# Kernel tuning notes

Measured on AMD Instinct MI355X. Metric: run time of the kernel, lower is better.

The kernel has to match this reference:

```python
import jax, jax.numpy as jnp
import numpy as np
from jax import lax

RADIUS = 0.15
K = 32          # num_neighbors
S = 1024        # num_centers
GROUPS = 8      # GroupNorm groups
EPS = 1e-5


def furthest_point_sample(xyz, n_samples):
    # xyz: [B, N, 3] -> indices [B, n_samples] (sequential FPS, start at index 0)
    B, N, _ = xyz.shape
    def step(carry, _):
        min_d, far = carry                      # [B,N], [B]
        sel = jnp.take_along_axis(xyz, far[:, None, None], axis=1)  # [B,1,3]
        d = jnp.sum((xyz - sel) ** 2, axis=-1)  # [B,N]
        min_d = jnp.minimum(min_d, d)
        nxt = jnp.argmax(min_d, axis=-1).astype(jnp.int32)
        return (min_d, nxt), far
    init = (jnp.full((B, N), jnp.inf, dtype=xyz.dtype), jnp.zeros((B,), jnp.int32))
    _, idxs = lax.scan(step, init, None, length=n_samples)  # [n_samples, B]
    return idxs.T  # [B, n_samples]


def ball_query(centers, points, radius, k):
    # centers: [B,3,S], points: [B,3,N] -> neighbor indices [B,S,k]
    B = points.shape[0]
    N = points.shape[-1]
    d2 = jnp.sum((centers[:, :, :, None] - points[:, :, None, :]) ** 2, axis=1)  # [B,S,N]
    valid = d2 < radius * radius
    order = jnp.where(valid, jnp.arange(N, dtype=jnp.int32), jnp.int32(N))
    topk = jnp.sort(order, axis=-1)[..., :k]            # first-k in-ball indices (CUDA ball_query order)
    first = topk[..., :1]
    idx = jnp.where(topk < N, topk, first)              # pad shortfall with first in-ball point
    idx = jnp.where(idx == N, 0, idx)                   # empty ball -> index 0
    return idx


def grouping(x, idx):
    # x: [B,C,N], idx: [B,S,k] -> [B,C,S,k]
    B, C, N = x.shape
    _, s, k = idx.shape
    flat = idx.reshape(B, 1, s * k)
    g = jnp.take_along_axis(x, jnp.broadcast_to(flat, (B, C, s * k)), axis=2)
    return g.reshape(B, C, s, k)


def group_norm(x, gamma, beta):
    # x: [B,C,S,K], GroupNorm(GROUPS)
    B, C, s, k = x.shape
    xg = x.reshape(B, GROUPS, C // GROUPS, s, k)
    mu = jnp.mean(xg, axis=(2, 3, 4), keepdims=True)
    var = jnp.var(xg, axis=(2, 3, 4), keepdims=True)
    xn = ((xg - mu) * lax.rsqrt(var + EPS)).reshape(B, C, s, k)
    return xn * gamma[None, :, None, None] + beta[None, :, None, None]


def mlp_layer(x, w, b, gamma, beta):
    # 1x1 Conv2d + GroupNorm + swish; x: [B,C,S,K], w: [O,C]
    y = jnp.einsum('bcsk,oc->bosk', x, w) + b[None, :, None, None]
    y = group_norm(y, gamma, beta)
    return y * jax.nn.sigmoid(y)


def setup_inputs() -> dict:
    key = jax.random.key(0)
    ks = jax.random.split(key, 20)
    B, C_IN, N = 8, 128, 4096
    features = jax.random.normal(ks[0], (B, C_IN, N), jnp.float32)
    coords = jax.random.uniform(ks[1], (B, 3, N), jnp.float32)
    time_emb = jax.random.normal(ks[2], (B, 64, N), jnp.float32)
    style = jax.random.normal(ks[3], (B, 64), jnp.float32)
    chans = [C_IN + 3, 128, 128, 256]
    inp = dict(features=features, coords=coords, time_emb=time_emb, style=style)
    for i in range(3):
        ci, co = chans[i], chans[i + 1]
        inp[f'w{i+1}'] = jax.random.normal(ks[4 + 4 * i], (co, ci), jnp.float32) / np.sqrt(ci)
        inp[f'b{i+1}'] = jnp.zeros((co,), jnp.float32)
        inp[f'g{i+1}'] = jnp.ones((co,), jnp.float32)
        inp[f'be{i+1}'] = jnp.zeros((co,), jnp.float32)
    return inp


def reference(features, coords, time_emb, style,
              w1, b1, g1, be1, w2, b2, g2, be2, w3, b3, g3, be3):
    # FPS -> center coords
    fps_idx = furthest_point_sample(coords.transpose(0, 2, 1), S)       # [B,S]
    B = coords.shape[0]
    centers = jnp.take_along_axis(coords, jnp.broadcast_to(fps_idx[:, None, :], (B, 3, S)), axis=2)  # [B,3,S]
    # Ball query + grouping (include_coordinates=True)
    nidx = ball_query(centers, coords, RADIUS, K)                       # [B,S,K]
    ncoords = grouping(coords, nidx) - centers[:, :, :, None]           # [B,3,S,K]
    nfeat = jnp.concatenate([ncoords, grouping(features, nidx)], axis=1)  # [B,3+C,S,K]
    # SharedMLP (1x1 conv + GN(8) + swish) x3, then max over neighbors
    x = mlp_layer(nfeat, w1, b1, g1, be1)
    x = mlp_layer(x, w2, b2, g2, be2)
    x = mlp_layer(x, w3, b3, g3, be3)
    out = jnp.max(x, axis=-1)                                           # [B,256,S]
    return out, centers, time_emb[:, :, :S], style
```

## Files before the change

kernel.cpp:

```cpp
#include <hip/hip_runtime.h>
#include <hip/hip_bf16.h>

#define BATCH 8
#define NPTS 4096
#define NS   1024
#define NK   32
#define CIN  128
#define C1PAD 160
#define O1   128
#define O3   256
#define MTOT 32768
#define GN_EPS 1e-5f

typedef float f32x4 __attribute__((ext_vector_type(4)));
typedef float f32x2 __attribute__((ext_vector_type(2)));
typedef short s16x8 __attribute__((ext_vector_type(8)));
typedef short s16x4 __attribute__((ext_vector_type(4)));
typedef unsigned long long u64;
typedef u64 u64x2 __attribute__((ext_vector_type(2)));

static __device__ __forceinline__ unsigned short f2bf(float f){
  unsigned u = __float_as_uint(f);
  u += 0x7fffu + ((u >> 16) & 1u);
  return (unsigned short)(u >> 16);
}
static __device__ __forceinline__ float bf2f(unsigned short h){
  return __uint_as_float(((unsigned)h) << 16);
}
static __device__ __forceinline__ float exact_d2(float ax,float ay,float az,float bx,float by,float bz){
  float dx=__fadd_rn(ax,-bx), dy=__fadd_rn(ay,-by), dz=__fadd_rn(az,-bz);
  return __fadd_rn(__fadd_rn(__fmul_rn(dx,dx),__fmul_rn(dy,dy)),__fmul_rn(dz,dz));
}
static __device__ __forceinline__ unsigned wave_umax_dpp(unsigned v){
  unsigned o;
  o = (unsigned)__builtin_amdgcn_update_dpp(0, (int)v, 0x111, 0xf, 0xf, true); v = (o>v)?o:v;
  o = (unsigned)__builtin_amdgcn_update_dpp(0, (int)v, 0x112, 0xf, 0xf, true); v = (o>v)?o:v;
  o = (unsigned)__builtin_amdgcn_update_dpp(0, (int)v, 0x114, 0xf, 0xf, true); v = (o>v)?o:v;
  o = (unsigned)__builtin_amdgcn_update_dpp(0, (int)v, 0x118, 0xf, 0xf, true); v = (o>v)?o:v;
  o = (unsigned)__builtin_amdgcn_update_dpp(0, (int)v, 0x142, 0xf, 0xf, true); v = (o>v)?o:v;
  o = (unsigned)__builtin_amdgcn_update_dpp(0, (int)v, 0x143, 0xf, 0xf, true); v = (o>v)?o:v;
  return v;
}
static __device__ __forceinline__ float wave_fsum_dpp(float v){
  int o;
  o=__builtin_amdgcn_update_dpp(0,__float_as_int(v),0x111,0xf,0xf,true); v+=__int_as_float(o);
  o=__builtin_amdgcn_update_dpp(0,__float_as_int(v),0x112,0xf,0xf,true); v+=__int_as_float(o);
  o=__builtin_amdgcn_update_dpp(0,__float_as_int(v),0x114,0xf,0xf,true); v+=__int_as_float(o);
  o=__builtin_amdgcn_update_dpp(0,__float_as_int(v),0x118,0xf,0xf,true); v+=__int_as_float(o);
  o=__builtin_amdgcn_update_dpp(0,__float_as_int(v),0x142,0xf,0xf,true); v+=__int_as_float(o);
  o=__builtin_amdgcn_update_dpp(0,__float_as_int(v),0x143,0xf,0xf,true); v+=__int_as_float(o);
  return v;
}
static __device__ __forceinline__ float fast_sigmoid(float x){
  return __builtin_amdgcn_rcpf(1.0f + __expf(-x));
}

#define FPS_BLOCKS 8
#define FT_BASE    8
#define FT_BLOCKS  128
#define ZP_BASE    136
#define ZP_BLOCKS  8
#define WP_BASE    144
#define WP_BLOCKS  36
#define MS_BASE    180
#define MS_BLOCKS  32
#define TOTAL_BLOCKS 212

__global__ __launch_bounds__(256) void k_fused(
    const float* __restrict__ coords, const float* __restrict__ features,
    const float* __restrict__ time_emb, const float* __restrict__ style,
    const float* __restrict__ w1, const float* __restrict__ w2, const float* __restrict__ w3,
    float* __restrict__ centers, float* __restrict__ out_time, float* __restrict__ out_style,
    unsigned short* __restrict__ featT, unsigned short* __restrict__ wfrag,
    float* __restrict__ stats){
  union U {
    struct { float4 lc[NPTS];
             unsigned long long red[2][4] __attribute__((aligned(16))); } fps;
    float tile[64][65];
  };
  __shared__ U sm;
  const int blk = blockIdx.x;
  const int t = threadIdx.x;

  if(blk < FPS_BLOCKS){
    const int b = blk;
    const float* cb = coords + (size_t)b*3*NPTS;
    const int lane = t & 63, wid = t >> 6;
    f32x2 px2[8],py2[8],pz2[8],md2[8];
    #pragma unroll
    for(int i=0;i<8;++i){
      int p0 = t + (2*i)*256;
      px2[i]=(f32x2){cb[p0],cb[p0+256]};
      py2[i]=(f32x2){cb[NPTS+p0],cb[NPTS+p0+256]};
      pz2[i]=(f32x2){cb[2*NPTS+p0],cb[2*NPTS+p0+256]};
      md2[i]=(f32x2){3.4e38f,3.4e38f};
      sm.fps.lc[p0]     = make_float4(px2[i].x, py2[i].x, pz2[i].x, 0.f);
      sm.fps.lc[p0+256] = make_float4(px2[i].y, py2[i].y, pz2[i].y, 0.f);
    }
    float ax=cb[0], ay=cb[NPTS], az=cb[2*NPTS];
    if(t==0){
      centers[(size_t)(b*3+0)*NS]=ax;
      centers[(size_t)(b*3+1)*NS]=ay;
      centers[(size_t)(b*3+2)*NS]=az;
    }
    __syncthreads();
    for(int it=1; it<NS; ++it){
      {
        #pragma clang fp contract(off)
        f32x2 axv={ax,ax}, ayv={ay,ay}, azv={az,az};
        #pragma unroll
        for(int i=0;i<8;++i){
          f32x2 dx=px2[i]-axv, dy=py2[i]-ayv, dz=pz2[i]-azv;
          f32x2 d = dx*dx + dy*dy + dz*dz;
          md2[i].x=fminf(md2[i].x,d.x);
          md2[i].y=fminf(md2[i].y,d.y);
        }
      }
      float m[8];
      #pragma unroll
      for(int i=0;i<8;++i) m[i]=fmaxf(md2[i].x,md2[i].y);
      float bmax=fmaxf(fmaxf(fmaxf(m[0],m[1]),fmaxf(m[2],m[3])),
                       fmaxf(fmaxf(m[4],m[5]),fmaxf(m[6],m[7])));
      unsigned bvb=(unsigned)__builtin_amdgcn_readlane((int)wave_umax_dpp(__float_as_uint(bmax)),63);
      unsigned cand=0u;
      #pragma unroll
      for(int s=15;s>=0;--s){
        float mv = (s&1)? md2[s>>1].y : md2[s>>1].x;
        cand = (__float_as_uint(mv)==bvb) ? ~(unsigned)(s*256+t) : cand;
      }
      unsigned mc = wave_umax_dpp(cand);
      const int buf=it&1;
      if(lane==63) sm.fps.red[buf][wid] = ((u64)bvb<<32) | mc;
      __syncthreads();
      u64x2 r0 = *(const u64x2*)&sm.fps.red[buf][0];
      u64x2 r1 = *(const u64x2*)&sm.fps.red[buf][2];
      u64 a0 = r0.x>r0.y?r0.x:r0.y;
      u64 a1 = r1.x>r1.y?r1.x:r1.y;
      u64 w  = a0>a1?a0:a1;
      unsigned idx = ~(unsigned)w;
      float4 c4 = sm.fps.lc[idx];
      ax=c4.x; ay=c4.y; az=c4.z;
      if(t==0){
        centers[(size_t)(b*3+0)*NS+it]=ax;
        centers[(size_t)(b*3+1)*NS+it]=ay;
        centers[(size_t)(b*3+2)*NS+it]=az;
      }
    }
    return;
  }

  if(blk < ZP_BASE){
    const int pb = blk - FT_BASE;
    for(int j=0;j<8;++j){
      int tid = pb*8 + j;
      int bb = tid>>7, r = tid&127, ct = r>>6, pt = r&63;
      int c0 = ct*64, p0 = pt*64;
      #pragma unroll
      for(int i=0;i<16;++i){
        int c = (t>>6)*16 + i;
        sm.tile[c][t&63] = features[((size_t)bb*CIN + c0 + c)*NPTS + p0 + (t&63)];
      }
      __syncthreads();
      #pragma unroll
      for(int i=0;i<16;++i){
        int pl = (t>>6)*16 + i;
        featT[((size_t)bb*NPTS + p0 + pl)*C1PAD + c0 + (t&63)] = f2bf(sm.tile[t&63][pl]);
      }
      __syncthreads();
    }
    return;
  }

  if(blk < WP_BASE){
    const int zb = blk - ZP_BASE;
    s16x8 z = (s16x8){0,0,0,0,0,0,0,0};
    #pragma unroll 4
    for(int i=0;i<64;++i){
      int q = zb*16384 + i*256 + t;
      int bb = q>>14, rem = q&16383, r = rem>>2, c8 = (rem&3)*8;
      *(s16x8*)&featT[((size_t)bb*NPTS + r)*C1PAD + 128 + c8] = z;
    }
    return;
  }

  if(blk < MS_BASE){
    int task = (blk - WP_BASE)*256 + t;
    if(task >= 9088) return;
    if(task >= 8704){
      int z = task - 8704;
      if(z < 3*BATCH*8*2) stats[z] = 0.f;
      return;
    }
    int layer, of, cs, ln, ncs; size_t base;
    if(task < 2560){ layer=0; ncs=5; base=0;     int r=task;      of=r/320; r%=320; cs=r>>6; ln=r&63; }
    else if(task < 4608){ layer=1; ncs=4; base=20480; int r=task-2560; of=r>>8; r&=255; cs=r>>6; ln=r&63; }
    else { layer=2; ncs=4; base=36864; int r=task-4608; of=r>>8; r&=255; cs=r>>6; ln=r&63; }
    int o = of*16 + (ln&15);
    s16x8 vals;
    #pragma unroll
    for(int i=0;i<8;++i){
      int c = cs*32 + (ln>>4)*8 + i;
      float v = 0.f;
      if(layer==0){
        if(c<128) v = w1[o*131 + c + 3];
        else if(c<131) v = w1[o*131 + (c-128)];
      } else if(layer==1){
        if(c<128) v = w2[o*128 + c];
      } else {
        if(c<128) v = w3[o*128 + c];
      }
      vals[i]=(short)f2bf(v);
    }
    *(s16x8*)&wfrag[base + ((size_t)(of*ncs + cs)*64 + ln)*8] = vals;
    return;
  }

  {
    const int mb = blk - MS_BASE;
    #pragma unroll 4
    for(int i=0;i<16;++i){
      int q = mb*4096 + i*256 + t;
      int f = q*4;
      int bb = f>>16, c = (f>>10)&63, s = f&1023;
      *(float4*)&out_time[f] = *(const float4*)&time_emb[((size_t)bb*64 + c)*NPTS + s];
    }
    if(mb==0){ out_style[t]=style[t]; out_style[256+t]=style[256+t]; }
  }
}

__global__ __launch_bounds__(256) void k_ballq(const float* __restrict__ coords,
                                               const float* __restrict__ centers,
                                               int* __restrict__ nidx){
  const int gw = (blockIdx.x*256 + threadIdx.x) >> 6;
  const int lane = threadIdx.x & 63;
  const int wl = (threadIdx.x >> 6);
  const int b = gw >> 10, s = gw & (NS-1);
  const float* cb = coords + (size_t)b*3*NPTS;
  const float cx = centers[(size_t)(b*3+0)*NS+s];
  const float cy = centers[(size_t)(b*3+1)*NS+s];
  const float cz = centers[(size_t)(b*3+2)*NS+s];
  __shared__ int slots[4][NK];
  int cnt = 0;
  for(int base=0; base<NPTS && cnt<NK; base+=64){
    int p = base + lane;
    float d2 = exact_d2(cb[p], cb[NPTS+p], cb[2*NPTS+p], cx,cy,cz);
    bool valid = d2 < 0.0225f;
    unsigned long long mask = __ballot(valid);
    int pos = cnt + (int)__popcll(mask & ((1ull<<lane)-1ull));
    if(valid && pos < NK) slots[wl][pos] = p;
    cnt += (int)__popcll(mask);
  }
  __syncthreads();
  int first = slots[wl][0];
  if(lane < NK){
    int v = (lane < cnt) ? slots[wl][lane] : first;
    nidx[((size_t)b*NS + s)*NK + lane] = v;
  }
}

__global__ __launch_bounds__(256) void k_gemm1(const unsigned short* __restrict__ featT,
    const int* __restrict__ nidx, const float* __restrict__ coords,
    const float* __restrict__ centers, const unsigned short* __restrict__ wfrag,
    const float* __restrict__ bias, unsigned short* __restrict__ yout,
    float* __restrict__ stats){
  const int b=blockIdx.y, mt=blockIdx.x;
  const int m0=mt*64;
  const int t=threadIdx.x, lane=t&63, wid=t>>6;
  __shared__ unsigned short xs[64][168];
  __shared__ unsigned short ys[64][136];
  __shared__ int pidx[64];
  __shared__ float cenS[2][3];
  __shared__ float wsum[2][8][4];
  if(t<64) pidx[t]=nidx[(size_t)b*MTOT + m0 + t];
  if(t>=64 && t<70){ int u=t-64; int j=u/3, c=u%3; cenS[j][c]=centers[((size_t)b*3+c)*NS + (m0>>5)+j]; }
  __syncthreads();
  for(int q=t;q<1280;q+=256){
    int r=q&63, ch=q>>6;
    *(s16x8*)&xs[r][ch*8] = *(const s16x8*)&featT[((size_t)b*NPTS + pidx[r])*C1PAD + ch*8];
  }
  __syncthreads();
  if(t<64){
    int p=pidx[t]; int sj=t>>5;
    float n0=__fadd_rn(coords[((size_t)b*3+0)*NPTS+p],-cenS[sj][0]);
    float n1=__fadd_rn(coords[((size_t)b*3+1)*NPTS+p],-cenS[sj][1]);
    float n2=__fadd_rn(coords[((size_t)b*3+2)*NPTS+p],-cenS[sj][2]);
    s16x4 nc={(short)f2bf(n0),(short)f2bf(n1),(short)f2bf(n2),0};
    *(s16x4*)&xs[t][128]=nc;
  }
  __syncthreads();
  f32x4 acc[8];
  #pragma unroll
  for(int i=0;i<8;++i) acc[i]=(f32x4){0.f,0.f,0.f,0.f};
  const unsigned short* xrow=&xs[wid*16+(lane&15)][0];
  #pragma unroll
  for(int cs=0;cs<5;++cs){
    s16x8 bfv=*(const s16x8*)&xrow[cs*32+(lane>>4)*8];
    #pragma unroll
    for(int of=0;of<8;++of){
      s16x8 afv=*(const s16x8*)&wfrag[((size_t)(of*5+cs)*64+lane)*8];
      acc[of]=__builtin_amdgcn_mfma_f32_16x16x32_bf16(afv,bfv,acc[of],0,0,0);
    }
  }
  #pragma unroll
  for(int of=0;of<8;++of){
    float ls=0.f,lq=0.f;
    int obase=of*16+((lane>>4)<<2);
    #pragma unroll
    for(int r=0;r<4;++r){
      float y=acc[of][r]+bias[obase+r];
      ys[wid*16+(lane&15)][obase+r]=f2bf(y);
      ls+=y; lq+=y*y;
    }
    ls=wave_fsum_dpp(ls); lq=wave_fsum_dpp(lq);
    if(lane==63){ wsum[0][of][wid]=ls; wsum[1][of][wid]=lq; }
  }
  __syncthreads();
  for(int q=t;q<1024;q+=256){
    int r=q&63, ch=q>>6;
    *(s16x8*)&yout[((size_t)b*MTOT+m0+r)*O1 + ch*8] = *(const s16x8*)&ys[r][ch*8];
  }
  if(t<8){
    float s1v=wsum[0][t][0]+wsum[0][t][1]+wsum[0][t][2]+wsum[0][t][3];
    float s2v=wsum[1][t][0]+wsum[1][t][1]+wsum[1][t][2]+wsum[1][t][3];
    atomicAdd(&stats[((0*BATCH+b)*8+t)*2+0],s1v);
    atomicAdd(&stats[((0*BATCH+b)*8+t)*2+1],s2v);
  }
}

template<int LAYER>
__global__ __launch_bounds__(256) void k_gemm23(const unsigned short* __restrict__ xin,
    const unsigned short* __restrict__ wfrag, const float* __restrict__ bias,
    const float* __restrict__ stats, const float* __restrict__ gprev,
    const float* __restrict__ beprev, unsigned short* __restrict__ yout,
    float* __restrict__ ymm, float* __restrict__ statsOut){
  const int b=blockIdx.y, mt=blockIdx.x;
  const int m0=mt*64;
  const int t=threadIdx.x, lane=t&63, wid=t>>6;
  __shared__ unsigned short xs[64][136];
  __shared__ unsigned short ys[64][136];
  __shared__ float lsc[CIN], lsh[CIN];
  __shared__ float wsum[2][8][4];
  if(t<CIN){
    int g = t>>4;
    const float cnt = 16.0f*NS*NK;
    float s1=stats[(((LAYER-1)*BATCH+b)*8+g)*2+0];
    float s2=stats[(((LAYER-1)*BATCH+b)*8+g)*2+1];
    float mu=s1/cnt, var=s2/cnt-mu*mu;
    float sc=gprev[t]*rsqrtf(var+GN_EPS);
    lsc[t]=sc; lsh[t]=beprev[t]-mu*sc;
  }
  __syncthreads();
  for(int q=t;q<1024;q+=256){
    int r=q&63, ch=q>>6;
    s16x8 v = *(const s16x8*)&xin[((size_t)b*MTOT + m0 + r)*CIN + ch*8];
    s16x8 o;
    #pragma unroll
    for(int i=0;i<8;++i){
      int c=ch*8+i;
      float x = bf2f((unsigned short)v[i]);
      x = x*lsc[c] + lsh[c];
      o[i]=(short)f2bf(x*fast_sigmoid(x));
    }
    *(s16x8*)&xs[r][ch*8]=o;
  }
  __syncthreads();
  const unsigned short* xrow=&xs[wid*16+(lane&15)][0];
  s16x8 bfv[4];
  #pragma unroll
  for(int cs=0;cs<4;++cs) bfv[cs]=*(const s16x8*)&xrow[cs*32+(lane>>4)*8];
  const int NPH=(LAYER==2)?2:1;
  #pragma unroll
  for(int ph=0; ph<NPH; ++ph){
    f32x4 acc[8];
    #pragma unroll
    for(int i=0;i<8;++i) acc[i]=(f32x4){0.f,0.f,0.f,0.f};
    #pragma unroll
    for(int cs=0;cs<4;++cs){
      #pragma unroll
      for(int of=0;of<8;++of){
        int ofg=ph*8+of;
        s16x8 afv=*(const s16x8*)&wfrag[((size_t)(ofg*4+cs)*64+lane)*8];
        acc[of]=__builtin_amdgcn_mfma_f32_16x16x32_bf16(afv,bfv[cs],acc[of],0,0,0);
      }
    }
    #pragma unroll
    for(int of=0;of<8;++of){
      float ls=0.f,lq=0.f;
      int lobase=of*16+((lane>>4)<<2);
      #pragma unroll
      for(int r=0;r<4;++r){
        float y=acc[of][r]+bias[ph*128+lobase+r];
        ys[wid*16+(lane&15)][lobase+r]=f2bf(y);
        ls+=y; lq+=y*y;
      }
      ls=wave_fsum_dpp(ls); lq=wave_fsum_dpp(lq);
      if(lane==63){ wsum[0][of][wid]=ls; wsum[1][of][wid]=lq; }
    }
    __syncthreads();
    if constexpr(LAYER==1){
      for(int q=t;q<1024;q+=256){
        int r=q&63, ch=q>>6;
        *(s16x8*)&yout[((size_t)b*MTOT+m0+r)*O1 + ch*8] = *(const s16x8*)&ys[r][ch*8];
      }
    } else {
      int c = t&127, sg = t>>7;
      float mn=3.4e38f, mx=-3.4e38f;
      #pragma unroll 8
      for(int k=0;k<32;++k){
        float v = bf2f(ys[sg*32+k][c]);
        mn=fminf(mn,v); mx=fmaxf(mx,v);
      }
      *(float2*)&ymm[(((size_t)b*NS + mt*2 + sg)*512) + (size_t)(ph*128+c)*2] = make_float2(mn,mx);
    }
    if(t<8){
      float s1v=wsum[0][t][0]+wsum[0][t][1]+wsum[0][t][2]+wsum[0][t][3];
      float s2v=wsum[1][t][0]+wsum[1][t][1]+wsum[1][t][2]+wsum[1][t][3];
      int g = (LAYER==2) ? (ph*4 + (t>>1)) : t;
      atomicAdd(&statsOut[((LAYER*BATCH+b)*8+g)*2+0],s1v);
      atomicAdd(&statsOut[((LAYER*BATCH+b)*8+g)*2+1],s2v);
    }
    if(ph+1<NPH) __syncthreads();
  }
}

__global__ __launch_bounds__(256) void k_out(const float* __restrict__ ymm,
    const float* __restrict__ stats, const float* __restrict__ g3,
    const float* __restrict__ be3, float* __restrict__ out){
  const int b=blockIdx.z, st=blockIdx.x;
  const int t=threadIdx.x;
  __shared__ float outT[256][33];
  const int c=t, g=c>>5;
  const float cnt = 32.0f*NS*NK;
  float s1=stats[((2*BATCH+b)*8+g)*2+0];
  float s2=stats[((2*BATCH+b)*8+g)*2+1];
  float mu=s1/cnt, var=s2/cnt-mu*mu;
  float sc=g3[c]*rsqrtf(var+GN_EPS);
  float sh=be3[c]-mu*sc;
  for(int si=0;si<32;++si){
    int s=st*32+si;
    float2 v=*(const float2*)&ymm[((size_t)b*NS+s)*512 + (size_t)c*2];
    float za=v.x*sc+sh, zb=v.y*sc+sh;
    float fa=za*fast_sigmoid(za);
    float fb=zb*fast_sigmoid(zb);
    outT[c][si]=fmaxf(fa,fb);
  }
  __syncthreads();
  #pragma unroll
  for(int i=0;i<32;++i){
    int row=(t>>5)+i*8;
    out[((size_t)(b*256+row))*NS + st*32 + (t&31)] = outT[row][t&31];
  }
}

extern "C" void kernel_launch(void* const* d_in, const int* in_sizes, int n_in,
                              void* d_out, int out_size, void* d_ws, size_t ws_size,
                              hipStream_t stream){
  const float* features=(const float*)d_in[0];
  const float* coords=(const float*)d_in[1];
  const float* time_emb=(const float*)d_in[2];
  const float* style=(const float*)d_in[3];
  const float* w1=(const float*)d_in[4];
  const float* b1=(const float*)d_in[5];
  const float* g1=(const float*)d_in[6];
  const float* be1=(const float*)d_in[7];
  const float* w2=(const float*)d_in[8];
  const float* b2=(const float*)d_in[9];
  const float* g2=(const float*)d_in[10];
  const float* be2=(const float*)d_in[11];
  const float* w3=(const float*)d_in[12];
  const float* b3=(const float*)d_in[13];
  const float* g3=(const float*)d_in[14];
  const float* be3=(const float*)d_in[15];

  float* out0=(float*)d_out;
  float* out_centers=out0 + (size_t)BATCH*O3*NS;
  float* out_time=out_centers + (size_t)BATCH*3*NS;
  float* out_style=out_time + (size_t)BATCH*64*NS;

  char* ws=(char*)d_ws;
  int* nidx=(int*)(ws + 131072);
  unsigned short* featT=(unsigned short*)(ws + 1179648);
  unsigned short* wfrag=(unsigned short*)(ws + 11796480);
  float* stats=(float*)(ws + 11939840);
  float* ymm=(float*)(ws + 12582912);
  unsigned short* y1=(unsigned short*)(ws + 33554432);
  unsigned short* y2=(unsigned short*)(ws + 100663296);

  k_fused<<<TOTAL_BLOCKS,256,0,stream>>>(coords,features,time_emb,style,w1,w2,w3,
                                         out_centers,out_time,out_style,featT,wfrag,stats);
  k_ballq<<<2048,256,0,stream>>>(coords,out_centers,nidx);
  k_gemm1<<<dim3(512,BATCH),256,0,stream>>>(featT,nidx,coords,out_centers,wfrag,b1,y1,stats);
  k_gemm23<1><<<dim3(512,BATCH),256,0,stream>>>(y1,wfrag+20480,b2,stats,g1,be1,y2,ymm,stats);
  k_gemm23<2><<<dim3(512,BATCH),256,0,stream>>>(y2,wfrag+36864,b3,stats,g2,be2,y2,ymm,stats);
  k_out<<<dim3(32,1,BATCH),256,0,stream>>>(ymm,stats,g3,be3,out0);
}
```

Baseline: 1.051 ms.

## Fuse ball query into GEMM1, DPP min/max in layer 3, vectorize FPS min/max

The standalone ball-query kernel is removed. Two waves of each GEMM1 block now run the neighbor search for their own two centers and write the indices straight into shared memory, which drops a kernel launch and the global round trip for the index buffer. In layer 3, the per-neighbor min/max is computed with 16-lane DPP reductions on register values instead of writing bf16 tiles to LDS and scanning 32 rows. The FPS loop also switches to packed 2-wide elementwise min/max. The cost is that half the waves in each GEMM1 block do serial ball-query work while the other two wait at the barrier.

```diff
diff --git a/kernel.cpp b/kernel.cpp
--- a/kernel.cpp
+++ b/kernel.cpp
@@ -49,6 +49,22 @@
   o=__builtin_amdgcn_update_dpp(0,__float_as_int(v),0x118,0xf,0xf,true); v+=__int_as_float(o);
   o=__builtin_amdgcn_update_dpp(0,__float_as_int(v),0x142,0xf,0xf,true); v+=__int_as_float(o);
   o=__builtin_amdgcn_update_dpp(0,__float_as_int(v),0x143,0xf,0xf,true); v+=__int_as_float(o);
+  return v;
+}
+static __device__ __forceinline__ float grp16_fmin_dpp(float v){
+  int o;
+  o=__builtin_amdgcn_update_dpp(0,__float_as_int(v),0x111,0xf,0xf,true); v=fminf(v,__int_as_float(o));
+  o=__builtin_amdgcn_update_dpp(0,__float_as_int(v),0x112,0xf,0xf,true); v=fminf(v,__int_as_float(o));
+  o=__builtin_amdgcn_update_dpp(0,__float_as_int(v),0x114,0xf,0xf,true); v=fminf(v,__int_as_float(o));
+  o=__builtin_amdgcn_update_dpp(0,__float_as_int(v),0x118,0xf,0xf,true); v=fminf(v,__int_as_float(o));
+  return v;
+}
+static __device__ __forceinline__ float grp16_fmax_dpp(float v){
+  int o;
+  o=__builtin_amdgcn_update_dpp(0,__float_as_int(v),0x111,0xf,0xf,true); v=fmaxf(v,__int_as_float(o));
+  o=__builtin_amdgcn_update_dpp(0,__float_as_int(v),0x112,0xf,0xf,true); v=fmaxf(v,__int_as_float(o));
+  o=__builtin_amdgcn_update_dpp(0,__float_as_int(v),0x114,0xf,0xf,true); v=fmaxf(v,__int_as_float(o));
+  o=__builtin_amdgcn_update_dpp(0,__float_as_int(v),0x118,0xf,0xf,true); v=fmaxf(v,__int_as_float(o));
   return v;
 }
 static __device__ __forceinline__ float fast_sigmoid(float x){
@@ -112,15 +128,17 @@
         for(int i=0;i<8;++i){
           f32x2 dx=px2[i]-axv, dy=py2[i]-ayv, dz=pz2[i]-azv;
           f32x2 d = dx*dx + dy*dy + dz*dz;
-          md2[i].x=fminf(md2[i].x,d.x);
-          md2[i].y=fminf(md2[i].y,d.y);
+          md2[i]=__builtin_elementwise_min(md2[i],d);
         }
       }
-      float m[8];
-      #pragma unroll
-      for(int i=0;i<8;++i) m[i]=fmaxf(md2[i].x,md2[i].y);
-      float bmax=fmaxf(fmaxf(fmaxf(m[0],m[1]),fmaxf(m[2],m[3])),
-                       fmaxf(fmaxf(m[4],m[5]),fmaxf(m[6],m[7])));
+      f32x2 t01=__builtin_elementwise_max(md2[0],md2[1]);
+      f32x2 t23=__builtin_elementwise_max(md2[2],md2[3]);
+      f32x2 t45=__builtin_elementwise_max(md2[4],md2[5]);
+      f32x2 t67=__builtin_elementwise_max(md2[6],md2[7]);
+      f32x2 ta=__builtin_elementwise_max(t01,t23);
+      f32x2 tb=__builtin_elementwise_max(t45,t67);
+      f32x2 tc=__builtin_elementwise_max(ta,tb);
+      float bmax=fmaxf(tc.x,tc.y);
       unsigned bvb=(unsigned)__builtin_amdgcn_readlane((int)wave_umax_dpp(__float_as_uint(bmax)),63);
       unsigned cand=0u;
       #pragma unroll
@@ -228,41 +246,10 @@
   }
 }
 
-__global__ __launch_bounds__(256) void k_ballq(const float* __restrict__ coords,
-                                               const float* __restrict__ centers,
-                                               int* __restrict__ nidx){
-  const int gw = (blockIdx.x*256 + threadIdx.x) >> 6;
-  const int lane = threadIdx.x & 63;
-  const int wl = (threadIdx.x >> 6);
-  const int b = gw >> 10, s = gw & (NS-1);
-  const float* cb = coords + (size_t)b*3*NPTS;
-  const float cx = centers[(size_t)(b*3+0)*NS+s];
-  const float cy = centers[(size_t)(b*3+1)*NS+s];
-  const float cz = centers[(size_t)(b*3+2)*NS+s];
-  __shared__ int slots[4][NK];
-  int cnt = 0;
-  for(int base=0; base<NPTS && cnt<NK; base+=64){
-    int p = base + lane;
-    float d2 = exact_d2(cb[p], cb[NPTS+p], cb[2*NPTS+p], cx,cy,cz);
-    bool valid = d2 < 0.0225f;
-    unsigned long long mask = __ballot(valid);
-    int pos = cnt + (int)__popcll(mask & ((1ull<<lane)-1ull));
-    if(valid && pos < NK) slots[wl][pos] = p;
-    cnt += (int)__popcll(mask);
-  }
-  __syncthreads();
-  int first = slots[wl][0];
-  if(lane < NK){
-    int v = (lane < cnt) ? slots[wl][lane] : first;
-    nidx[((size_t)b*NS + s)*NK + lane] = v;
-  }
-}
-
 __global__ __launch_bounds__(256) void k_gemm1(const unsigned short* __restrict__ featT,
-    const int* __restrict__ nidx, const float* __restrict__ coords,
-    const float* __restrict__ centers, const unsigned short* __restrict__ wfrag,
-    const float* __restrict__ bias, unsigned short* __restrict__ yout,
-    float* __restrict__ stats){
+    const float* __restrict__ coords, const float* __restrict__ centers,
+    const unsigned short* __restrict__ wfrag, const float* __restrict__ bias,
+    unsigned short* __restrict__ yout, float* __restrict__ stats){
   const int b=blockIdx.y, mt=blockIdx.x;
   const int m0=mt*64;
   const int t=threadIdx.x, lane=t&63, wid=t>>6;
@@ -271,8 +258,29 @@
   __shared__ int pidx[64];
   __shared__ float cenS[2][3];
   __shared__ float wsum[2][8][4];
-  if(t<64) pidx[t]=nidx[(size_t)b*MTOT + m0 + t];
-  if(t>=64 && t<70){ int u=t-64; int j=u/3, c=u%3; cenS[j][c]=centers[((size_t)b*3+c)*NS + (m0>>5)+j]; }
+  if(wid<2){
+    const int s0=(m0>>5)+wid;
+    const float cx=centers[(size_t)(b*3+0)*NS+s0];
+    const float cy=centers[(size_t)(b*3+1)*NS+s0];
+    const float cz=centers[(size_t)(b*3+2)*NS+s0];
+    if(lane==0){ cenS[wid][0]=cx; cenS[wid][1]=cy; cenS[wid][2]=cz; }
+    const float* cb=coords+(size_t)b*3*NPTS;
+    int cnt=0;
+    for(int base=0;base<NPTS&&cnt<NK;base+=64){
+      int p=base+lane;
+      float d2=exact_d2(cb[p],cb[NPTS+p],cb[2*NPTS+p],cx,cy,cz);
+      bool valid=d2<0.0225f;
+      unsigned long long mask=__ballot(valid);
+      int pos=cnt+(int)__popcll(mask&((1ull<<lane)-1ull));
+      if(valid&&pos<NK) pidx[wid*32+pos]=p;
+      cnt+=(int)__popcll(mask);
+    }
+    int first=pidx[wid*32];
+    if(lane<NK){
+      int v=(lane<cnt)?pidx[wid*32+lane]:first;
+      pidx[wid*32+lane]=v;
+    }
+  }
   __syncthreads();
   for(int q=t;q<1280;q+=256){
     int r=q&63, ch=q>>6;
@@ -337,7 +345,7 @@
   const int m0=mt*64;
   const int t=threadIdx.x, lane=t&63, wid=t>>6;
   __shared__ unsigned short xs[64][136];
-  __shared__ unsigned short ys[64][136];
+  __shared__ union SY { unsigned short ys[64][136]; float2 part[4][128]; } sy;
   __shared__ float lsc[CIN], lsh[CIN];
   __shared__ float wsum[2][8][4];
   if(t<CIN){
@@ -387,11 +395,27 @@
     for(int of=0;of<8;++of){
       float ls=0.f,lq=0.f;
       int lobase=of*16+((lane>>4)<<2);
-      #pragma unroll
-      for(int r=0;r<4;++r){
-        float y=acc[of][r]+bias[ph*128+lobase+r];
-        ys[wid*16+(lane&15)][lobase+r]=f2bf(y);
-        ls+=y; lq+=y*y;
+      if constexpr(LAYER==1){
+        #pragma unroll
+        for(int r=0;r<4;++r){
+          float y=acc[of][r]+bias[lobase+r];
+          sy.ys[wid*16+(lane&15)][lobase+r]=f2bf(y);
+          ls+=y; lq+=y*y;
+        }
+      } else {
+        float mnv[4], mxv[4];
+        #pragma unroll
+        for(int r=0;r<4;++r){
+          float y=acc[of][r]+bias[ph*128+lobase+r];
+          ls+=y; lq+=y*y;
+          float yr=bf2f(f2bf(y));
+          mnv[r]=grp16_fmin_dpp(yr);
+          mxv[r]=grp16_fmax_dpp(yr);
+        }
+        if((lane&15)==15){
+          #pragma unroll
+          for(int r=0;r<4;++r) sy.part[wid][lobase+r]=make_float2(mnv[r],mxv[r]);
+        }
       }
       ls=wave_fsum_dpp(ls); lq=wave_fsum_dpp(lq);
       if(lane==63){ wsum[0][of][wid]=ls; wsum[1][of][wid]=lq; }
@@ -400,17 +424,13 @@
     if constexpr(LAYER==1){
       for(int q=t;q<1024;q+=256){
         int r=q&63, ch=q>>6;
-        *(s16x8*)&yout[((size_t)b*MTOT+m0+r)*O1 + ch*8] = *(const s16x8*)&ys[r][ch*8];
+        *(s16x8*)&yout[((size_t)b*MTOT+m0+r)*O1 + ch*8] = *(const s16x8*)&sy.ys[r][ch*8];
       }
     } else {
       int c = t&127, sg = t>>7;
-      float mn=3.4e38f, mx=-3.4e38f;
-      #pragma unroll 8
-      for(int k=0;k<32;++k){
-        float v = bf2f(ys[sg*32+k][c]);
-        mn=fminf(mn,v); mx=fmaxf(mx,v);
-      }
-      *(float2*)&ymm[(((size_t)b*NS + mt*2 + sg)*512) + (size_t)(ph*128+c)*2] = make_float2(mn,mx);
+      float2 pa=sy.part[sg*2][c], pb=sy.part[sg*2+1][c];
+      *(float2*)&ymm[(((size_t)b*NS + mt*2 + sg)*512) + (size_t)(ph*128+c)*2]
+          = make_float2(fminf(pa.x,pb.x), fmaxf(pa.y,pb.y));
     }
     if(t<8){
       float s1v=wsum[0][t][0]+wsum[0][t][1]+wsum[0][t][2]+wsum[0][t][3];
@@ -478,7 +498,6 @@
   float* out_style=out_time + (size_t)BATCH*64*NS;
 
   char* ws=(char*)d_ws;
-  int* nidx=(int*)(ws + 131072);
   unsigned short* featT=(unsigned short*)(ws + 1179648);
   unsigned short* wfrag=(unsigned short*)(ws + 11796480);
   float* stats=(float*)(ws + 11939840);
@@ -488,8 +507,7 @@
 
   k_fused<<<TOTAL_BLOCKS,256,0,stream>>>(coords,features,time_emb,style,w1,w2,w3,
                                          out_centers,out_time,out_style,featT,wfrag,stats);
-  k_ballq<<<2048,256,0,stream>>>(coords,out_centers,nidx);
-  k_gemm1<<<dim3(512,BATCH),256,0,stream>>>(featT,nidx,coords,out_centers,wfrag,b1,y1,stats);
+  k_gemm1<<<dim3(512,BATCH),256,0,stream>>>(featT,coords,out_centers,wfrag,b1,y1,stats);
   k_gemm23<1><<<dim3(512,BATCH),256,0,stream>>>(y1,wfrag+20480,b2,stats,g1,be1,y2,ymm,stats);
   k_gemm23<2><<<dim3(512,BATCH),256,0,stream>>>(y2,wfrag+36864,b3,stats,g2,be2,y2,ymm,stats);
   k_out<<<dim3(32,1,BATCH),256,0,stream>>>(ymm,stats,g3,be3,out0);
```

Result: slower. 1.151 ms (+9.5%).
